# Performance work log

Hardware: AMD Instinct MI355X
Metric: run time of the kernel (lower is better)

The kernel has to match this reference:

```python
import jax, jax.numpy as jnp
import numpy as np

EMBED = 768
HEADS = 12
HEAD_DIM = EMBED // HEADS
HIDDEN = 3072
PATCH = 16
IMG = 224
GRID = IMG // PATCH  # 14
NP = GRID * GRID     # 196 patches per image
N_IMAGES = 4
N_BLOCKS = N_IMAGES - 1
B = 8


def layernorm(x, g, b, eps=1e-5):
    mu = jnp.mean(x, axis=-1, keepdims=True)
    var = jnp.mean(jnp.square(x - mu), axis=-1, keepdims=True)
    return (x - mu) * jax.lax.rsqrt(var + eps) * g + b


def patch_embed(img, w, bias):
    # conv2d(k=patch, stride=patch) == unfold to patches + linear
    Bn = img.shape[0]
    x = img.reshape(Bn, 3, GRID, PATCH, GRID, PATCH)
    x = x.transpose(0, 2, 4, 1, 3, 5).reshape(Bn, NP, 3 * PATCH * PATCH)
    return x @ w.reshape(EMBED, -1).T + bias  # [B, NP, EMBED]


def setup_inputs() -> dict:
    key = jax.random.key(0)
    ks = iter(jax.random.split(key, 64))
    d = {}
    for i in range(N_IMAGES):
        d[f"img{i}"] = jax.random.normal(next(ks), (B, 3, IMG, IMG), jnp.float32)
    d["pe_w"] = jax.random.normal(next(ks), (N_IMAGES, EMBED, 3, PATCH, PATCH)) * 0.02
    d["pe_b"] = jnp.zeros((N_IMAGES, EMBED))
    d["spatial_pos"] = jax.random.normal(next(ks), (1, NP, EMBED // 2))
    d["image_pos"] = jax.random.normal(next(ks), (1, N_IMAGES, EMBED // 2))
    d["ln_attn_g"] = jnp.ones((N_BLOCKS, EMBED)); d["ln_attn_b"] = jnp.zeros((N_BLOCKS, EMBED))
    d["qkv_w"] = jax.random.normal(next(ks), (N_BLOCKS, 3 * EMBED, EMBED)) * 0.02
    d["qkv_b"] = jnp.zeros((N_BLOCKS, 3 * EMBED))
    d["proj_w"] = jax.random.normal(next(ks), (N_BLOCKS, EMBED, EMBED)) * 0.02
    d["proj_b"] = jnp.zeros((N_BLOCKS, EMBED))
    d["ln1_g"] = jnp.ones((N_BLOCKS, EMBED)); d["ln1_b"] = jnp.zeros((N_BLOCKS, EMBED))
    d["fc1_w"] = jax.random.normal(next(ks), (N_BLOCKS, HIDDEN, EMBED)) * 0.02
    d["fc1_b"] = jnp.zeros((N_BLOCKS, HIDDEN))
    d["fc2_w"] = jax.random.normal(next(ks), (N_BLOCKS, EMBED, HIDDEN)) * 0.02
    d["fc2_b"] = jnp.zeros((N_BLOCKS, EMBED))
    d["ln2_g"] = jnp.ones((N_BLOCKS, EMBED)); d["ln2_b"] = jnp.zeros((N_BLOCKS, EMBED))
    d["final_g"] = jnp.ones((EMBED,)); d["final_b"] = jnp.zeros((EMBED,))
    d["head_w1"] = jax.random.normal(next(ks), (EMBED, EMBED)) * 0.02
    d["head_b1"] = jnp.zeros((EMBED,))
    d["head_w2"] = jax.random.normal(next(ks), (PATCH * PATCH, EMBED)) * 0.02
    d["head_b2"] = jnp.zeros((PATCH * PATCH,))
    return d


def _pos_encode(x, spatial_pos, image_pos, img_idx):
    n = x.shape[1]
    sp = spatial_pos[:, :n, :]                       # [1, n, E/2]
    ip = jnp.broadcast_to(image_pos[:, img_idx:img_idx + 1, :], (1, n, EMBED // 2))
    return x + jnp.concatenate([sp, ip], axis=-1)


def _block(x, i, p):
    # pre-norm + manual MHA
    residual = x
    h = layernorm(x, p["ln_attn_g"][i], p["ln_attn_b"][i])
    Bn, N, C = h.shape
    qkv = (h @ p["qkv_w"][i].T + p["qkv_b"][i]).reshape(Bn, N, 3, HEADS, HEAD_DIM)
    q, k, v = (qkv[:, :, j].transpose(0, 2, 1, 3) for j in range(3))  # [B,H,N,d]
    attn = jax.nn.softmax(jnp.einsum("bhnd,bhmd->bhnm", q, k) * HEAD_DIM ** -0.5, axis=-1)
    o = jnp.einsum("bhnm,bhmd->bhnd", attn, v).transpose(0, 2, 1, 3).reshape(Bn, N, C)
    x = residual + (o @ p["proj_w"][i].T + p["proj_b"][i])
    # conv block (1x1 convs == linear over channel dim)
    r = x
    h = layernorm(x, p["ln1_g"][i], p["ln1_b"][i])
    h = jax.nn.gelu(h @ p["fc1_w"][i].T + p["fc1_b"][i], approximate=False)
    h = h @ p["fc2_w"][i].T + p["fc2_b"][i]
    return layernorm(r + h, p["ln2_g"][i], p["ln2_b"][i])


def reference(img0, img1, img2, img3, pe_w, pe_b, spatial_pos, image_pos,
              ln_attn_g, ln_attn_b, qkv_w, qkv_b, proj_w, proj_b,
              ln1_g, ln1_b, fc1_w, fc1_b, fc2_w, fc2_b, ln2_g, ln2_b,
              final_g, final_b, head_w1, head_b1, head_w2, head_b2):
    p = dict(ln_attn_g=ln_attn_g, ln_attn_b=ln_attn_b, qkv_w=qkv_w, qkv_b=qkv_b,
             proj_w=proj_w, proj_b=proj_b, ln1_g=ln1_g, ln1_b=ln1_b,
             fc1_w=fc1_w, fc1_b=fc1_b, fc2_w=fc2_w, fc2_b=fc2_b,
             ln2_g=ln2_g, ln2_b=ln2_b)
    images = [img0, img1, img2, img3]
    x1 = _pos_encode(patch_embed(images[0], pe_w[0], pe_b[0]), spatial_pos, image_pos, 0)
    x2 = _pos_encode(patch_embed(images[1], pe_w[1], pe_b[1]), spatial_pos, image_pos, 1)
    x = jnp.concatenate([x1, x2], axis=1)
    x = _block(x, 0, p)
    for i in range(2, N_IMAGES):
        xn = _pos_encode(patch_embed(images[i], pe_w[i], pe_b[i]), spatial_pos, image_pos, i)
        x = jnp.concatenate([x, xn], axis=1)
        x = _block(x, i - 1, p)
    x = layernorm(x, final_g, final_b)
    x = jnp.mean(x, axis=1)                                  # [B, E]
    h = jax.nn.gelu(x @ head_w1.T + head_b1, approximate=False)
    patches = h @ head_w2.T + head_b2                        # [B, PATCH*PATCH]
    Bn = patches.shape[0]
    pimg = patches.reshape(Bn, 1, PATCH, PATCH, 1, 1)
    pimg = jnp.broadcast_to(pimg, (Bn, 1, PATCH, PATCH, GRID, GRID))
    out = pimg.transpose(0, 1, 4, 2, 5, 3).reshape(Bn, 1, IMG, IMG)
    return out
```

## Files before the change

### kernel.cpp

```cpp
#include <hip/hip_runtime.h>
#include <hip/hip_bf16.h>
#include <math.h>

#define EMBED 768
#define QKVD 2304
#define HEADS 12
#define HD 64
#define HIDDEN 3072
#define NPATCH 196
#define SEQMAX 784
#define NB 8
#define IMGSZ 224
#define GRID 14
#define PATCH 16
#define PSTR 72
#define VROW 832

typedef __hip_bfloat16 bf16;
typedef __attribute__((ext_vector_type(8))) short short8;
typedef __attribute__((ext_vector_type(4))) float f32x4;

__device__ __forceinline__ float b2f(bf16 v) { return __bfloat162float(v); }
__device__ __forceinline__ float geluf(float x) {
    return 0.5f * x * (1.0f + erff(x * 0.70710678118654752f));
}

__device__ __forceinline__ void async16(const bf16* g, bf16* l) {
    __builtin_amdgcn_global_load_lds(
        (const __attribute__((address_space(1))) unsigned int*)g,
        (__attribute__((address_space(3))) unsigned int*)l,
        16, 0, 0);
}

#define WAIT_VM0   0x0F70
#define WAIT_VM3   0x0F73
#define WAIT_VM4   0x0F74
#define WAIT_VM5   0x0F75
#define WAIT_VM6   0x0F76
#define WAIT_LGKM0 0xC07F

__global__ __launch_bounds__(256)
void detect_kernel(const unsigned short* __restrict__ raw, int* __restrict__ flag)
{
    __shared__ int bad;
    if (threadIdx.x == 0) bad = 0;
    __syncthreads();
    for (int i = threadIdx.x; i < 8192; i += 256) {
        unsigned int u = (unsigned int)raw[i] << 16;
        float v = __uint_as_float(u);
        if (!(fabsf(v) <= 1e4f)) bad = 1;
    }
    __syncthreads();
    if (threadIdx.x == 0) *flag = bad;
}

struct CvtF32 {
    const void* src[19];
    int n[19];
    int dstOff[19];
    int blkOff[20];
};
__global__ __launch_bounds__(256)
void convert_f32_all(CvtF32 c, float* __restrict__ base, const int* __restrict__ flag)
{
    int f = *flag;
    int b = blockIdx.x;
    int i = 0;
    #pragma unroll
    for (int j = 0; j < 19; ++j) if (b >= c.blkOff[j + 1]) i = j + 1;
    int e = ((b - c.blkOff[i]) * 256 + threadIdx.x) * 4;
    if (e >= c.n[i]) return;
    float* dst = base + c.dstOff[i] + e;
    if (f) {
        *(float4*)dst = *(const float4*)((const float*)c.src[i] + e);
    } else {
        const bf16* s = (const bf16*)c.src[i] + e;
        dst[0] = b2f(s[0]); dst[1] = b2f(s[1]); dst[2] = b2f(s[2]); dst[3] = b2f(s[3]);
    }
}

struct CvtB16 {
    const void* src[5];
    int n[5];
    int dstOff[5];
    int blkOff[6];
};
__global__ __launch_bounds__(256)
void convert_b16_all(CvtB16 c, bf16* __restrict__ base, const int* __restrict__ flag)
{
    int f = *flag;
    int b = blockIdx.x;
    int i = 0;
    #pragma unroll
    for (int j = 0; j < 5; ++j) if (b >= c.blkOff[j + 1]) i = j + 1;
    int e = ((b - c.blkOff[i]) * 256 + threadIdx.x) * 4;
    if (e >= c.n[i]) return;
    bf16* dst = base + (size_t)c.dstOff[i] + e;
    if (f) {
        float4 v = *(const float4*)((const float*)c.src[i] + e);
        dst[0] = __float2bfloat16(v.x); dst[1] = __float2bfloat16(v.y);
        dst[2] = __float2bfloat16(v.z); dst[3] = __float2bfloat16(v.w);
    } else {
        *(uint2*)dst = *(const uint2*)((const bf16*)c.src[i] + e);
    }
}

template<int MT>
__global__ __launch_bounds__(256)
void mfma_gemm(const bf16* __restrict__ A, const bf16* __restrict__ W,
               const float* __restrict__ bias, const float* __restrict__ add,
               float* __restrict__ outF, bf16* __restrict__ outB,
               bf16* __restrict__ Qb, bf16* __restrict__ Kb, bf16* __restrict__ Vb,
               int M, int N, int K, int Ntok, int rowStride, int mode, int magic)
{
    constexpr int MI = MT / 32;
    __shared__ __align__(16) bf16 As[2][MT * 32];
    __shared__ __align__(16) bf16 Bs[3][128 * 32];
    int tid = threadIdx.x;
    int lane = tid & 63;
    int wave = tid >> 6;
    int wm = wave & 1, wn = wave >> 1;
    int m0 = blockIdx.y * MT, n0 = blockIdx.x * 128;

    int lr = lane >> 2;
    int lc = lane & 3;
    int sc = lc ^ ((lr >> 1) & 3);
    int ar0 = (MT / 4) * wave + lr;
    int ma0 = m0 + ar0; if (ma0 >= M) ma0 = M - 1;
    int bx0 = (int)(((unsigned)ma0 * (unsigned)magic) >> 24);
    const bf16* aSrc0 = A + (size_t)(bx0 * rowStride + (ma0 - bx0 * Ntok)) * K + sc * 8;
    const bf16* aSrc1 = nullptr;
    if constexpr (MT == 128) {
        int ma1 = m0 + ar0 + 16; if (ma1 >= M) ma1 = M - 1;
        int bx1 = (int)(((unsigned)ma1 * (unsigned)magic) >> 24);
        aSrc1 = A + (size_t)(bx1 * rowStride + (ma1 - bx1 * Ntok)) * K + sc * 8;
    }
    const bf16* bSrc0 = W + (size_t)(n0 + 32 * wave + lr) * K + sc * 8;
    const bf16* bSrc1 = W + (size_t)(n0 + 32 * wave + 16 + lr) * K + sc * 8;

    int fr = lane & 15;
    int fq = lane >> 4;
    int sq = fq ^ ((fr >> 1) & 3);
    int aOff = (wm * (MT / 2) + fr) * 32 + sq * 8;
    int bOff = (wn * 64 + fr) * 32 + sq * 8;

    f32x4 acc[MI][4] = {};

    auto stageA = [&](int buf) {
        async16(aSrc0, As[buf] + ((MT / 4) * wave) * 32);
        aSrc0 += 32;
        if constexpr (MT == 128) {
            async16(aSrc1, As[buf] + ((MT / 4) * wave + 16) * 32);
            aSrc1 += 32;
        }
    };
    auto stageB = [&](int buf) {
        async16(bSrc0, Bs[buf] + (32 * wave) * 32);
        async16(bSrc1, Bs[buf] + (32 * wave + 16) * 32);
        bSrc0 += 32; bSrc1 += 32;
    };

    int nIter = K >> 5;
    stageB(0);
    stageA(0);
    stageB(1);

    int cur = 0;
    for (int it = 0; it < nIter; ++it) {
        __builtin_amdgcn_sched_barrier(0);
        __builtin_amdgcn_s_waitcnt(WAIT_LGKM0);
        __builtin_amdgcn_s_barrier();
        if (it + 1 < nIter) stageA((it + 1) & 1);
        if (it + 2 < nIter) {
            int nb = cur + 2; if (nb >= 3) nb -= 3;
            stageB(nb);
            if constexpr (MT == 128) __builtin_amdgcn_s_waitcnt(WAIT_VM6);
            else                     __builtin_amdgcn_s_waitcnt(WAIT_VM5);
        } else if (it + 1 < nIter) {
            if constexpr (MT == 128) __builtin_amdgcn_s_waitcnt(WAIT_VM4);
            else                     __builtin_amdgcn_s_waitcnt(WAIT_VM3);
        } else {
            __builtin_amdgcn_s_waitcnt(WAIT_VM0);
        }
        __builtin_amdgcn_s_barrier();
        __builtin_amdgcn_sched_barrier(0);

        const bf16* aR = As[it & 1] + aOff;
        const bf16* bR = Bs[cur] + bOff;
        short8 af[MI], bfr[4];
        #pragma unroll
        for (int mi = 0; mi < MI; ++mi) af[mi] = *(const short8*)(aR + mi * 16 * 32);
        #pragma unroll
        for (int ni = 0; ni < 4; ++ni) bfr[ni] = *(const short8*)(bR + ni * 16 * 32);
        #pragma unroll
        for (int mi = 0; mi < MI; ++mi)
            #pragma unroll
            for (int ni = 0; ni < 4; ++ni)
                acc[mi][ni] = __builtin_amdgcn_mfma_f32_16x16x32_bf16(
                    af[mi], bfr[ni], acc[mi][ni], 0, 0, 0);
        if (++cur >= 3) cur = 0;
    }

    int prA[MI][4], bxA[MI][4], tA[MI][4];
    bool okA[MI][4];
    #pragma unroll
    for (int mi = 0; mi < MI; ++mi)
        #pragma unroll
        for (int r = 0; r < 4; ++r) {
            int m = m0 + wm * (MT / 2) + mi * 16 + fq * 4 + r;
            okA[mi][r] = (m < M);
            if (m >= M) m = M - 1;
            int bx = (int)(((unsigned)m * (unsigned)magic) >> 24);
            int t = m - bx * Ntok;
            bxA[mi][r] = bx; tA[mi][r] = t;
            prA[mi][r] = bx * rowStride + t;
        }

    float bsv[4];
    #pragma unroll
    for (int ni = 0; ni < 4; ++ni) bsv[ni] = bias[n0 + wn * 64 + ni * 16 + fr];

    if (mode == 3) {
        #pragma unroll
        for (int ni = 0; ni < 4; ++ni) {
            int nb = n0 + wn * 64 + ni * 16;
            int which = (nb >= 1536) ? 2 : (nb >= 768) ? 1 : 0;
            int nnb = nb - which * 768;
            int hh = nnb >> 6;
            int dcol = (nnb & 63) + fr;
            bf16* dstb = (which == 0) ? Qb : (which == 1) ? Kb : Vb;
            #pragma unroll
            for (int mi = 0; mi < MI; ++mi)
                #pragma unroll
                for (int r = 0; r < 4; ++r) {
                    if (!okA[mi][r]) continue;
                    float v = acc[mi][ni][r] + bsv[ni];
                    dstb[((size_t)(bxA[mi][r] * HEADS + hh) * SEQMAX + tA[mi][r]) * HD + dcol]
                        = __float2bfloat16(v);
                }
        }
    } else {
        #pragma unroll
        for (int mi = 0; mi < MI; ++mi)
            #pragma unroll
            for (int r = 0; r < 4; ++r) {
                if (!okA[mi][r]) continue;
                size_t rb = (size_t)prA[mi][r] * N;
                #pragma unroll
                for (int ni = 0; ni < 4; ++ni) {
                    int n = n0 + wn * 64 + ni * 16 + fr;
                    float v = acc[mi][ni][r] + bsv[ni];
                    if (mode == 0)      outF[rb + n] = v;
                    else if (mode == 1) outF[rb + n] = v + add[rb + n];
                    else                outB[rb + n] = __float2bfloat16(geluf(v));
                }
            }
    }
}

__global__ __launch_bounds__(256)
void gemm_kernel(const float* __restrict__ A, const float* __restrict__ W,
                 const float* __restrict__ bias, const float* __restrict__ add,
                 float* __restrict__ C, int M, int N, int K,
                 int Ntok, int rowStride, int dogelu)
{
    __shared__ __align__(16) float As[16][68];
    __shared__ __align__(16) float Ws[16][68];
    int tid = threadIdx.x;
    int tx = tid & 15, ty = tid >> 4;
    int n0 = blockIdx.x * 64, m0 = blockIdx.y * 64;
    int lrow = tid >> 2;
    int lk   = (tid & 3) << 2;
    int am = m0 + lrow;
    bool aok = (am < M);
    const float* Arow = A;
    if (aok) {
        int pr = (am / Ntok) * rowStride + (am % Ntok);
        Arow = A + (size_t)pr * K;
    }
    int wn = n0 + lrow;
    const float* Wrow = (wn < N) ? (W + (size_t)wn * K) : nullptr;
    float acc[4][4] = {};
    for (int kk = 0; kk < K; kk += 16) {
        float4 av = make_float4(0.f, 0.f, 0.f, 0.f);
        if (aok) av = *(const float4*)(Arow + kk + lk);
        float4 wv = make_float4(0.f, 0.f, 0.f, 0.f);
        if (Wrow) wv = *(const float4*)(Wrow + kk + lk);
        __syncthreads();
        As[lk+0][lrow] = av.x; As[lk+1][lrow] = av.y;
        As[lk+2][lrow] = av.z; As[lk+3][lrow] = av.w;
        Ws[lk+0][lrow] = wv.x; Ws[lk+1][lrow] = wv.y;
        Ws[lk+2][lrow] = wv.z; Ws[lk+3][lrow] = wv.w;
        __syncthreads();
        #pragma unroll
        for (int k = 0; k < 16; ++k) {
            float4 a = *(const float4*)&As[k][ty << 2];
            float4 w = *(const float4*)&Ws[k][tx << 2];
            acc[0][0] += a.x*w.x; acc[0][1] += a.x*w.y; acc[0][2] += a.x*w.z; acc[0][3] += a.x*w.w;
            acc[1][0] += a.y*w.x; acc[1][1] += a.y*w.y; acc[1][2] += a.y*w.z; acc[1][3] += a.y*w.w;
            acc[2][0] += a.z*w.x; acc[2][1] += a.z*w.y; acc[2][2] += a.z*w.z; acc[2][3] += a.z*w.w;
            acc[3][0] += a.w*w.x; acc[3][1] += a.w*w.y; acc[3][2] += a.w*w.z; acc[3][3] += a.w*w.w;
        }
    }
    #pragma unroll
    for (int i = 0; i < 4; ++i) {
        int m = m0 + (ty << 2) + i;
        if (m >= M) continue;
        int pr = (m / Ntok) * rowStride + (m % Ntok);
        float* crow = C + (size_t)pr * N;
        const float* addrow = add ? (add + (size_t)pr * N) : nullptr;
        #pragma unroll
        for (int j = 0; j < 4; ++j) {
            int n = n0 + (tx << 2) + j;
            float v = acc[i][j] + bias[n];
            if (addrow) v += addrow[n];
            if (dogelu) v = geluf(v);
            crow[n] = v;
        }
    }
}

__global__ __launch_bounds__(256)
void ln_bf16_kernel(const float* __restrict__ src, bf16* __restrict__ dst,
                    const float* __restrict__ g, const float* __restrict__ bta, int Ntok)
{
    __shared__ float red[256];
    int blk = blockIdx.x;
    int t = blk % Ntok, b = blk / Ntok;
    size_t row = ((size_t)b * SEQMAX + t) * EMBED;
    int tid = threadIdx.x;
    float v0 = src[row + tid], v1 = src[row + tid + 256], v2 = src[row + tid + 512];
    red[tid] = v0 + v1 + v2;
    __syncthreads();
    for (int off = 128; off; off >>= 1) { if (tid < off) red[tid] += red[tid + off]; __syncthreads(); }
    float mu = red[0] * (1.0f / EMBED);
    __syncthreads();
    float d0 = v0 - mu, d1 = v1 - mu, d2 = v2 - mu;
    red[tid] = d0*d0 + d1*d1 + d2*d2;
    __syncthreads();
    for (int off = 128; off; off >>= 1) { if (tid < off) red[tid] += red[tid + off]; __syncthreads(); }
    float rs = rsqrtf(red[0] * (1.0f / EMBED) + 1e-5f);
    dst[row + tid]       = __float2bfloat16(d0 * rs * g[tid]       + bta[tid]);
    dst[row + tid + 256] = __float2bfloat16(d1 * rs * g[tid + 256] + bta[tid + 256]);
    dst[row + tid + 512] = __float2bfloat16(d2 * rs * g[tid + 512] + bta[tid + 512]);
}

__global__ __launch_bounds__(256)
void ln_kernel(const float* __restrict__ src, float* __restrict__ dst,
               const float* __restrict__ g, const float* __restrict__ bta, int Ntok)
{
    __shared__ float red[256];
    int blk = blockIdx.x;
    int t = blk % Ntok, b = blk / Ntok;
    size_t row = ((size_t)b * SEQMAX + t) * EMBED;
    int tid = threadIdx.x;
    float v0 = src[row + tid], v1 = src[row + tid + 256], v2 = src[row + tid + 512];
    red[tid] = v0 + v1 + v2;
    __syncthreads();
    for (int off = 128; off; off >>= 1) { if (tid < off) red[tid] += red[tid + off]; __syncthreads(); }
    float mu = red[0] * (1.0f / EMBED);
    __syncthreads();
    float d0 = v0 - mu, d1 = v1 - mu, d2 = v2 - mu;
    red[tid] = d0*d0 + d1*d1 + d2*d2;
    __syncthreads();
    for (int off = 128; off; off >>= 1) { if (tid < off) red[tid] += red[tid + off]; __syncthreads(); }
    float rs = rsqrtf(red[0] * (1.0f / EMBED) + 1e-5f);
    dst[row + tid]       = d0 * rs * g[tid]       + bta[tid];
    dst[row + tid + 256] = d1 * rs * g[tid + 256] + bta[tid + 256];
    dst[row + tid + 512] = d2 * rs * g[tid + 512] + bta[tid + 512];
}

__global__ __launch_bounds__(256)
void vtrans_kernel(const bf16* __restrict__ Vh, bf16* __restrict__ VT, int Ntok)
{
    __shared__ unsigned short Lt[64 * 66];
    int bh = blockIdx.x;
    int k0 = blockIdx.y * 64;
    const bf16* Vb = Vh + (size_t)bh * SEQMAX * HD;
    int tid = threadIdx.x;
    #pragma unroll
    for (int pass = 0; pass < 8; ++pass) {
        int key_l = (tid >> 5) + pass * 8;
        int d2 = tid & 31;
        unsigned v = 0;
        if (k0 + key_l < Ntok)
            v = *(const unsigned*)(Vb + (size_t)(k0 + key_l) * HD + d2 * 2);
        *(unsigned*)&Lt[key_l * 66 + 2 * d2] = v;
    }
    __syncthreads();
    #pragma unroll
    for (int pass = 0; pass < 8; ++pass) {
        int d = (tid >> 5) + pass * 8;
        int kp = tid & 31;
        unsigned lo = Lt[(2 * kp) * 66 + d];
        unsigned hi = Lt[(2 * kp + 1) * 66 + d];
        *(unsigned*)(VT + ((size_t)bh * HD + d) * VROW + k0 + 2 * kp) = lo | (hi << 16);
    }
}

__global__ __launch_bounds__(256)
void flash_mfma(const bf16* __restrict__ Qh, const bf16* __restrict__ Kh,
                const bf16* __restrict__ VT, bf16* __restrict__ O, int Ntok)
{
    __shared__ __align__(16) unsigned short Plds[4][32 * PSTR];
    int bh = blockIdx.x;
    int b = bh / HEADS, h = bh % HEADS;
    int t0 = blockIdx.y * 128;
    int tid = threadIdx.x;
    int lane = tid & 63, w = tid >> 6;
    int fr = lane & 15, fq = lane >> 4;

    const bf16* Qb = Qh + (size_t)bh * SEQMAX * HD;
    const bf16* Kb = Kh + (size_t)bh * SEQMAX * HD;
    const bf16* Vt = VT + (size_t)bh * HD * VROW;

    short8 aq[2][2];
    #pragma unroll
    for (int qi = 0; qi < 2; ++qi) {
        int tq = t0 + w * 32 + qi * 16 + fr; if (tq >= Ntok) tq = Ntok - 1;
        aq[qi][0] = *(const short8*)(Qb + (size_t)tq * HD + fq * 8);
        aq[qi][1] = *(const short8*)(Qb + (size_t)tq * HD + fq * 8 + 32);
    }

    float lpart[2][4] = {};
    f32x4 oacc[2][4];
    #pragma unroll
    for (int qi = 0; qi < 2; ++qi)
        #pragma unroll
        for (int dg = 0; dg < 4; ++dg) oacc[qi][dg] = (f32x4){0.f, 0.f, 0.f, 0.f};

    unsigned short* Pw = Plds[w];

    for (int k0 = 0; k0 < Ntok; k0 += 64) {
        short8 bk[4][2];
        #pragma unroll
        for (int kg = 0; kg < 4; ++kg) {
            int key = k0 + kg * 16 + fr;
            int keyc = key < Ntok ? key : Ntok - 1;
            bk[kg][0] = *(const short8*)(Kb + (size_t)keyc * HD + fq * 8);
            bk[kg][1] = *(const short8*)(Kb + (size_t)keyc * HD + fq * 8 + 32);
        }
        short8 bv[4][2];
        #pragma unroll
        for (int dg = 0; dg < 4; ++dg) {
            int d = dg * 16 + fr;
            bv[dg][0] = *(const short8*)(Vt + (size_t)d * VROW + k0 + fq * 8);
            bv[dg][1] = *(const short8*)(Vt + (size_t)d * VROW + k0 + fq * 8 + 32);
        }

        float s[2][4][4];
        #pragma unroll
        for (int qi = 0; qi < 2; ++qi)
            #pragma unroll
            for (int kg = 0; kg < 4; ++kg) {
                f32x4 sa = (f32x4){0.f, 0.f, 0.f, 0.f};
                sa = __builtin_amdgcn_mfma_f32_16x16x32_bf16(aq[qi][0], bk[kg][0], sa, 0, 0, 0);
                sa = __builtin_amdgcn_mfma_f32_16x16x32_bf16(aq[qi][1], bk[kg][1], sa, 0, 0, 0);
                #pragma unroll
                for (int r = 0; r < 4; ++r) s[qi][kg][r] = sa[r];
            }

        #pragma unroll
        for (int qi = 0; qi < 2; ++qi)
            #pragma unroll
            for (int kg = 0; kg < 4; ++kg) {
                bool ok = (k0 + kg * 16 + fr) < Ntok;
                #pragma unroll
                for (int r = 0; r < 4; ++r) {
                    float p = ok ? __expf(fminf(s[qi][kg][r] * 0.125f, 80.f)) : 0.f;
                    lpart[qi][r] += p;
                    bf16 pb = __float2bfloat16(p);
                    Pw[(qi * 16 + fq * 4 + r) * PSTR + kg * 16 + fr] = *(unsigned short*)&pb;
                }
            }

        short8 ap[2][2];
        #pragma unroll
        for (int qi = 0; qi < 2; ++qi) {
            ap[qi][0] = *(const short8*)(Pw + (qi * 16 + fr) * PSTR + fq * 8);
            ap[qi][1] = *(const short8*)(Pw + (qi * 16 + fr) * PSTR + fq * 8 + 32);
        }

        #pragma unroll
        for (int qi = 0; qi < 2; ++qi)
            #pragma unroll
            for (int dg = 0; dg < 4; ++dg) {
                oacc[qi][dg] = __builtin_amdgcn_mfma_f32_16x16x32_bf16(
                    ap[qi][0], bv[dg][0], oacc[qi][dg], 0, 0, 0);
                oacc[qi][dg] = __builtin_amdgcn_mfma_f32_16x16x32_bf16(
                    ap[qi][1], bv[dg][1], oacc[qi][dg], 0, 0, 0);
            }
    }

    #pragma unroll
    for (int qi = 0; qi < 2; ++qi)
        #pragma unroll
        for (int r = 0; r < 4; ++r) {
            float l = lpart[qi][r];
            l += __shfl_xor(l, 1); l += __shfl_xor(l, 2);
            l += __shfl_xor(l, 4); l += __shfl_xor(l, 8);
            int t = t0 + w * 32 + qi * 16 + fq * 4 + r;
            if (t >= Ntok) continue;
            float inv = 1.0f / l;
            bf16* dst = O + ((size_t)b * SEQMAX + t) * EMBED + h * HD;
            #pragma unroll
            for (int dg = 0; dg < 4; ++dg)
                dst[dg * 16 + fr] = __float2bfloat16(oacc[qi][dg][r] * inv);
        }
}

__global__ __launch_bounds__(256)
void patch_gather(const void* __restrict__ img, bf16* __restrict__ Ap,
                  const int* __restrict__ flag)
{
    int f = *flag;
    int idx = blockIdx.x * 256 + threadIdx.x;
    if (idx >= NB * NPATCH * EMBED) return;
    int col = idx % EMBED;
    int row = idx / EMBED;
    int t = row % NPATCH, b = row / NPATCH;
    int c = col >> 8;
    int pr = (col >> 4) & 15;
    int pc = col & 15;
    int gr = t / GRID, gc = t % GRID;
    size_t off = ((size_t)(b * 3 + c) * IMGSZ + gr * PATCH + pr) * IMGSZ + gc * PATCH + pc;
    float v = f ? ((const float*)img)[off] : b2f(((const bf16*)img)[off]);
    Ap[idx] = __float2bfloat16(v);
}

__global__ __launch_bounds__(256)
void posadd_kernel(const float* __restrict__ PEO, const float* __restrict__ sp,
                   const float* __restrict__ ip, float* __restrict__ X, int imgIdx)
{
    int idx = blockIdx.x * 256 + threadIdx.x;
    if (idx >= NB * NPATCH * EMBED) return;
    int e = idx % EMBED;
    int row = idx / EMBED;
    int t = row % NPATCH, b = row / NPATCH;
    float pos = (e < 384) ? sp[t * 384 + e] : ip[imgIdx * 384 + (e - 384)];
    X[((size_t)b * SEQMAX + imgIdx * NPATCH + t) * EMBED + e] = PEO[idx] + pos;
}

__global__ __launch_bounds__(768)
void mean_kernel(const float* __restrict__ H, float* __restrict__ Mn)
{
    int b = blockIdx.x;
    int e = threadIdx.x;
    float s = 0.f;
    for (int t = 0; t < SEQMAX; ++t) s += H[((size_t)b * SEQMAX + t) * EMBED + e];
    Mn[b * EMBED + e] = s * (1.0f / SEQMAX);
}

__global__ __launch_bounds__(256)
void bcast_kernel(const float* __restrict__ P, void* __restrict__ out,
                  const int* __restrict__ flag)
{
    int f = *flag;
    int idx = blockIdx.x * 256 + threadIdx.x;
    if (idx >= NB * IMGSZ * IMGSZ) return;
    int c = idx % IMGSZ;
    int r = (idx / IMGSZ) % IMGSZ;
    int b = idx / (IMGSZ * IMGSZ);
    float v = P[b * 256 + (r & 15) * 16 + (c & 15)];
    if (f) ((float*)out)[idx] = v;
    else   ((bf16*)out)[idx] = __float2bfloat16(v);
}

extern "C" void kernel_launch(void* const* d_in, const int* in_sizes, int n_in,
                              void* d_out, int out_size, void* d_ws, size_t ws_size,
                              hipStream_t stream)
{
    (void)n_in; (void)out_size; (void)ws_size;
    const void* img[4] = {d_in[0], d_in[1], d_in[2], d_in[3]};

    float* ws = (float*)d_ws;
    int* flag = (int*)ws;

    detect_kernel<<<1, 256, 0, stream>>>((const unsigned short*)d_in[0], flag);

    const bool isBig[28] = {0,0,0,0, 1,0,0,0, 0,0,1,0, 1,0,0,0, 1,0,1,0, 0,0,0,0, 0,0,0,0};
    float* fBase = ws + 16;
    float* fPtr[28] = {};
    CvtF32 cf;
    int fCnt = 0, fBlk = 0;
    cf.blkOff[0] = 0;
    {
        float* p = fBase;
        for (int i = 4; i < 28; ++i) {
            if (isBig[i]) continue;
            fPtr[i] = p;
            int n = in_sizes[i];
            cf.src[fCnt] = d_in[i];
            cf.n[fCnt] = n;
            cf.dstOff[fCnt] = (int)(p - fBase);
            fBlk += (n + 1023) / 1024;
            cf.blkOff[fCnt + 1] = fBlk;
            p += n;
            ++fCnt;
        }
        fBase = ws + 16;
        fPtr[0] = p;
    }
    convert_f32_all<<<fBlk, 256, 0, stream>>>(cf, fBase, flag);

    bf16* bPtr[28] = {};
    bf16* bBase = (bf16*)fPtr[0];
    CvtB16 cb;
    int bCnt = 0, bBlk = 0;
    cb.blkOff[0] = 0;
    float* arenaEnd;
    {
        bf16* p = bBase;
        for (int i = 4; i < 28; ++i) {
            if (!isBig[i]) continue;
            bPtr[i] = p;
            int n = in_sizes[i];
            cb.src[bCnt] = d_in[i];
            cb.n[bCnt] = n;
            cb.dstOff[bCnt] = (int)(p - bBase);
            bBlk += (n + 1023) / 1024;
            cb.blkOff[bCnt + 1] = bBlk;
            p += n;
            ++bCnt;
        }
        size_t off = p - (bf16*)ws;
        off = (off + 7) & ~(size_t)7;
        arenaEnd = (float*)((bf16*)ws + off);
    }
    convert_b16_all<<<bBlk, 256, 0, stream>>>(cb, bBase, flag);

    const bf16* pe_w   = bPtr[4];
    const bf16* qkv_w  = bPtr[10];
    const bf16* proj_w = bPtr[12];
    const bf16* fc1_w  = bPtr[16];
    const bf16* fc2_w  = bPtr[18];
    const float* pe_b      = fPtr[5];
    const float* sp        = fPtr[6];
    const float* ip        = fPtr[7];
    const float* ln_attn_g = fPtr[8];
    const float* ln_attn_b = fPtr[9];
    const float* qkv_b     = fPtr[11];
    const float* proj_b    = fPtr[13];
    const float* ln1_g     = fPtr[14];
    const float* ln1_b     = fPtr[15];
    const float* fc1_b     = fPtr[17];
    const float* fc2_b     = fPtr[19];
    const float* ln2_g     = fPtr[20];
    const float* ln2_b     = fPtr[21];
    const float* final_g   = fPtr[22];
    const float* final_b   = fPtr[23];
    const float* head_w1   = fPtr[24];
    const float* head_b1   = fPtr[25];
    const float* head_w2   = fPtr[26];
    const float* head_b2   = fPtr[27];

    const size_t SEQ = (size_t)NB * SEQMAX * EMBED;
    const size_t HID_ELEMS = (size_t)NB * SEQMAX * HIDDEN;
    const size_t EMB_ELEMS = (size_t)NB * NPATCH * EMBED;
    float* X    = arenaEnd;
    float* H    = X + SEQ;
    float* O    = H + SEQ;
    float* PEO  = O + SEQ;
    float* MEAN = PEO + EMB_ELEMS;
    float* HH   = MEAN + NB * EMBED;
    float* PTCH = HH + NB * EMBED;
    bf16* Hb    = (bf16*)(PTCH + NB * 256 + 16);
    bf16* Ob    = Hb + SEQ;
    bf16* Gb    = Ob + SEQ;
    bf16* PEb   = Gb + HID_ELEMS;
    bf16* Qb    = PEb + EMB_ELEMS;
    bf16* Kb    = Qb + SEQ;
    bf16* Vb    = Kb + SEQ;
    bf16* VTb   = Vb + SEQ;

    const int nEmb = NB * NPATCH * EMBED;

    auto magicOf = [](int d) { return (int)(16777216u / (unsigned)d + 1u); };
    const int mgE = magicOf(NB * NPATCH);

    auto embed = [&](int i) {
        patch_gather<<<(nEmb + 255) / 256, 256, 0, stream>>>(img[i], PEb, flag);
        dim3 g(EMBED / 128, (NB * NPATCH + 63) / 64);
        mfma_gemm<64><<<g, 256, 0, stream>>>(PEb, pe_w + (size_t)i * EMBED * EMBED,
                                             pe_b + i * EMBED, nullptr, PEO, nullptr,
                                             nullptr, nullptr, nullptr,
                                             NB * NPATCH, EMBED, EMBED,
                                             NB * NPATCH, NB * NPATCH, 0, mgE);
        posadd_kernel<<<(nEmb + 255) / 256, 256, 0, stream>>>(PEO, sp, ip, X, i);
    };

    auto block = [&](int i, int Ntok) {
        int M = NB * Ntok;
        int gy64  = (M + 63) / 64;
        int nkt = (Ntok + 63) / 64;
        int nqt = (Ntok + 127) / 128;
        int mg = magicOf(Ntok);
        ln_bf16_kernel<<<M, 256, 0, stream>>>(X, Hb, ln_attn_g + i * EMBED, ln_attn_b + i * EMBED, Ntok);
        mfma_gemm<64><<<dim3(QKVD / 128, gy64), 256, 0, stream>>>(
            Hb, qkv_w + (size_t)i * QKVD * EMBED, qkv_b + i * QKVD, nullptr,
            nullptr, nullptr, Qb, Kb, Vb, M, QKVD, EMBED, Ntok, SEQMAX, 3, mg);
        vtrans_kernel<<<dim3(NB * HEADS, nkt), 256, 0, stream>>>(Vb, VTb, Ntok);
        flash_mfma<<<dim3(NB * HEADS, nqt), 256, 0, stream>>>(Qb, Kb, VTb, Ob, Ntok);
        mfma_gemm<64><<<dim3(EMBED / 128, gy64), 256, 0, stream>>>(
            Ob, proj_w + (size_t)i * EMBED * EMBED, proj_b + i * EMBED, X,
            X, nullptr, nullptr, nullptr, nullptr, M, EMBED, EMBED, Ntok, SEQMAX, 1, mg);
        ln_bf16_kernel<<<M, 256, 0, stream>>>(X, Hb, ln1_g + i * EMBED, ln1_b + i * EMBED, Ntok);
        mfma_gemm<64><<<dim3(HIDDEN / 128, gy64), 256, 0, stream>>>(
            Hb, fc1_w + (size_t)i * HIDDEN * EMBED, fc1_b + i * HIDDEN, nullptr,
            nullptr, Gb, nullptr, nullptr, nullptr, M, HIDDEN, EMBED, Ntok, SEQMAX, 2, mg);
        mfma_gemm<64><<<dim3(EMBED / 128, gy64), 256, 0, stream>>>(
            Gb, fc2_w + (size_t)i * EMBED * HIDDEN, fc2_b + i * EMBED, X,
            O, nullptr, nullptr, nullptr, nullptr, M, EMBED, HIDDEN, Ntok, SEQMAX, 1, mg);
        ln_kernel<<<M, 256, 0, stream>>>(O, X, ln2_g + i * EMBED, ln2_b + i * EMBED, Ntok);
    };

    embed(0);
    embed(1);
    block(0, 392);
    embed(2);
    block(1, 588);
    embed(3);
    block(2, 784);

    ln_kernel<<<NB * SEQMAX, 256, 0, stream>>>(X, H, final_g, final_b, SEQMAX);
    mean_kernel<<<NB, 768, 0, stream>>>(H, MEAN);
    gemm_kernel<<<dim3(EMBED / 64, 1), 256, 0, stream>>>(
        MEAN, head_w1, head_b1, nullptr, HH, NB, EMBED, EMBED, NB, NB, 1);
    gemm_kernel<<<dim3(256 / 64, 1), 256, 0, stream>>>(
        HH, head_w2, head_b2, nullptr, PTCH, NB, 256, EMBED, NB, NB, 0);
    bcast_kernel<<<(NB * IMGSZ * IMGSZ + 255) / 256, 256, 0, stream>>>(PTCH, d_out, flag);
}
```

Measured before the change: 1.284 ms.

## Split-K narrow GEMMs, XCD-aware block remap, 128-row tiles for wide GEMMs

```diff
diff --git a/kernel.cpp b/kernel.cpp
--- a/kernel.cpp
+++ b/kernel.cpp
@@ -106,12 +106,14 @@
 }
 
 template<int MT>
-__global__ __launch_bounds__(256)
+__global__ __launch_bounds__(256, 4)
 void mfma_gemm(const bf16* __restrict__ A, const bf16* __restrict__ W,
                const float* __restrict__ bias, const float* __restrict__ add,
-               float* __restrict__ outF, bf16* __restrict__ outB,
+               float* __restrict__ outF, float* __restrict__ outF2,
+               bf16* __restrict__ outB,
                bf16* __restrict__ Qb, bf16* __restrict__ Kb, bf16* __restrict__ Vb,
-               int M, int N, int K, int Ntok, int rowStride, int mode, int magic)
+               int M, int N, int K, int kpitch, int Ntok, int rowStride,
+               int mode, int magic)
 {
     constexpr int MI = MT / 32;
     __shared__ __align__(16) bf16 As[2][MT * 32];
@@ -120,7 +122,20 @@
     int lane = tid & 63;
     int wave = tid >> 6;
     int wm = wave & 1, wn = wave >> 1;
-    int m0 = blockIdx.y * MT, n0 = blockIdx.x * 128;
+
+    unsigned nx = gridDim.x, ny = gridDim.y;
+    unsigned nwg = nx * ny * gridDim.z;
+    unsigned orig = blockIdx.x + nx * (blockIdx.y + ny * blockIdx.z);
+    unsigned qq = nwg >> 3, rr = nwg & 7;
+    unsigned xcd = orig & 7, idx8 = orig >> 3;
+    unsigned wg = (xcd < rr ? xcd * (qq + 1) : rr * (qq + 1) + (xcd - rr) * qq) + idx8;
+    int bxg = (int)(wg % nx);
+    unsigned tmp = wg / nx;
+    int byg = (int)(tmp % ny);
+    int bzg = (int)(tmp / ny);
+
+    int m0 = byg * MT, n0 = bxg * 128;
+    int k0 = bzg * K;
 
     int lr = lane >> 2;
     int lc = lane & 3;
@@ -128,15 +143,15 @@
     int ar0 = (MT / 4) * wave + lr;
     int ma0 = m0 + ar0; if (ma0 >= M) ma0 = M - 1;
     int bx0 = (int)(((unsigned)ma0 * (unsigned)magic) >> 24);
-    const bf16* aSrc0 = A + (size_t)(bx0 * rowStride + (ma0 - bx0 * Ntok)) * K + sc * 8;
+    const bf16* aSrc0 = A + (size_t)(bx0 * rowStride + (ma0 - bx0 * Ntok)) * kpitch + k0 + sc * 8;
     const bf16* aSrc1 = nullptr;
     if constexpr (MT == 128) {
         int ma1 = m0 + ar0 + 16; if (ma1 >= M) ma1 = M - 1;
         int bx1 = (int)(((unsigned)ma1 * (unsigned)magic) >> 24);
-        aSrc1 = A + (size_t)(bx1 * rowStride + (ma1 - bx1 * Ntok)) * K + sc * 8;
-    }
-    const bf16* bSrc0 = W + (size_t)(n0 + 32 * wave + lr) * K + sc * 8;
-    const bf16* bSrc1 = W + (size_t)(n0 + 32 * wave + 16 + lr) * K + sc * 8;
+        aSrc1 = A + (size_t)(bx1 * rowStride + (ma1 - bx1 * Ntok)) * kpitch + k0 + sc * 8;
+    }
+    const bf16* bSrc0 = W + (size_t)(n0 + 32 * wave + lr) * kpitch + k0 + sc * 8;
+    const bf16* bSrc1 = W + (size_t)(n0 + 32 * wave + 16 + lr) * kpitch + k0 + sc * 8;
 
     int fr = lane & 15;
     int fq = lane >> 4;
@@ -201,57 +216,52 @@
         if (++cur >= 3) cur = 0;
     }
 
-    int prA[MI][4], bxA[MI][4], tA[MI][4];
-    bool okA[MI][4];
-    #pragma unroll
-    for (int mi = 0; mi < MI; ++mi)
-        #pragma unroll
-        for (int r = 0; r < 4; ++r) {
-            int m = m0 + wm * (MT / 2) + mi * 16 + fq * 4 + r;
-            okA[mi][r] = (m < M);
-            if (m >= M) m = M - 1;
-            int bx = (int)(((unsigned)m * (unsigned)magic) >> 24);
-            int t = m - bx * Ntok;
-            bxA[mi][r] = bx; tA[mi][r] = t;
-            prA[mi][r] = bx * rowStride + t;
-        }
-
+    float* oF = bzg ? outF2 : outF;
     float bsv[4];
     #pragma unroll
-    for (int ni = 0; ni < 4; ++ni) bsv[ni] = bias[n0 + wn * 64 + ni * 16 + fr];
+    for (int ni = 0; ni < 4; ++ni)
+        bsv[ni] = bzg ? 0.f : bias[n0 + wn * 64 + ni * 16 + fr];
 
     if (mode == 3) {
+        bf16* dstb[4]; int hhv[4], dcv[4];
         #pragma unroll
         for (int ni = 0; ni < 4; ++ni) {
             int nb = n0 + wn * 64 + ni * 16;
             int which = (nb >= 1536) ? 2 : (nb >= 768) ? 1 : 0;
             int nnb = nb - which * 768;
-            int hh = nnb >> 6;
-            int dcol = (nnb & 63) + fr;
-            bf16* dstb = (which == 0) ? Qb : (which == 1) ? Kb : Vb;
-            #pragma unroll
-            for (int mi = 0; mi < MI; ++mi)
-                #pragma unroll
-                for (int r = 0; r < 4; ++r) {
-                    if (!okA[mi][r]) continue;
-                    float v = acc[mi][ni][r] + bsv[ni];
-                    dstb[((size_t)(bxA[mi][r] * HEADS + hh) * SEQMAX + tA[mi][r]) * HD + dcol]
-                        = __float2bfloat16(v);
-                }
-        }
-    } else {
+            dstb[ni] = (which == 0) ? Qb : (which == 1) ? Kb : Vb;
+            hhv[ni] = nnb >> 6;
+            dcv[ni] = (nnb & 63) + fr;
+        }
         #pragma unroll
         for (int mi = 0; mi < MI; ++mi)
             #pragma unroll
             for (int r = 0; r < 4; ++r) {
-                if (!okA[mi][r]) continue;
-                size_t rb = (size_t)prA[mi][r] * N;
+                int m = m0 + wm * (MT / 2) + mi * 16 + fq * 4 + r;
+                if (m >= M) continue;
+                int bx_ = (int)(((unsigned)m * (unsigned)magic) >> 24);
+                int t = m - bx_ * Ntok;
+                #pragma unroll
+                for (int ni = 0; ni < 4; ++ni)
+                    dstb[ni][((size_t)(bx_ * HEADS + hhv[ni]) * SEQMAX + t) * HD + dcv[ni]]
+                        = __float2bfloat16(acc[mi][ni][r] + bsv[ni]);
+            }
+    } else {
+        #pragma unroll
+        for (int mi = 0; mi < MI; ++mi)
+            #pragma unroll
+            for (int r = 0; r < 4; ++r) {
+                int m = m0 + wm * (MT / 2) + mi * 16 + fq * 4 + r;
+                if (m >= M) continue;
+                int bx_ = (int)(((unsigned)m * (unsigned)magic) >> 24);
+                int t = m - bx_ * Ntok;
+                size_t rb = (size_t)(bx_ * rowStride + t) * N;
                 #pragma unroll
                 for (int ni = 0; ni < 4; ++ni) {
                     int n = n0 + wn * 64 + ni * 16 + fr;
                     float v = acc[mi][ni][r] + bsv[ni];
-                    if (mode == 0)      outF[rb + n] = v;
-                    else if (mode == 1) outF[rb + n] = v + add[rb + n];
+                    if (mode == 0)      oF[rb + n] = v;
+                    else if (mode == 1) oF[rb + n] = v + add[rb + n];
                     else                outB[rb + n] = __float2bfloat16(geluf(v));
                 }
             }
@@ -371,6 +381,34 @@
 }
 
 __global__ __launch_bounds__(256)
+void ln_sum_f32_kernel(const float* __restrict__ pa, const float* __restrict__ pb,
+                       float* __restrict__ X, const float* __restrict__ g,
+                       const float* __restrict__ bta, int Ntok)
+{
+    __shared__ float red[256];
+    int blk = blockIdx.x;
+    int t = blk % Ntok, b = blk / Ntok;
+    size_t row = ((size_t)b * SEQMAX + t) * EMBED;
+    int tid = threadIdx.x;
+    float v0 = pa[row + tid]       + pb[row + tid]       + X[row + tid];
+    float v1 = pa[row + tid + 256] + pb[row + tid + 256] + X[row + tid + 256];
+    float v2 = pa[row + tid + 512] + pb[row + tid + 512] + X[row + tid + 512];
+    red[tid] = v0 + v1 + v2;
+    __syncthreads();
+    for (int off = 128; off; off >>= 1) { if (tid < off) red[tid] += red[tid + off]; __syncthreads(); }
+    float mu = red[0] * (1.0f / EMBED);
+    __syncthreads();
+    float d0 = v0 - mu, d1 = v1 - mu, d2 = v2 - mu;
+    red[tid] = d0*d0 + d1*d1 + d2*d2;
+    __syncthreads();
+    for (int off = 128; off; off >>= 1) { if (tid < off) red[tid] += red[tid + off]; __syncthreads(); }
+    float rs = rsqrtf(red[0] * (1.0f / EMBED) + 1e-5f);
+    X[row + tid]       = d0 * rs * g[tid]       + bta[tid];
+    X[row + tid + 256] = d1 * rs * g[tid + 256] + bta[tid + 256];
+    X[row + tid + 512] = d2 * rs * g[tid + 512] + bta[tid + 512];
+}
+
+__global__ __launch_bounds__(256)
 void vtrans_kernel(const bf16* __restrict__ Vh, bf16* __restrict__ VT, int Ntok)
 {
     __shared__ unsigned short Lt[64 * 66];
@@ -529,8 +567,9 @@
 }
 
 __global__ __launch_bounds__(256)
-void posadd_kernel(const float* __restrict__ PEO, const float* __restrict__ sp,
-                   const float* __restrict__ ip, float* __restrict__ X, int imgIdx)
+void posadd_kernel(const float* __restrict__ PEO, const float* __restrict__ PEO2,
+                   const float* __restrict__ sp, const float* __restrict__ ip,
+                   float* __restrict__ X, int imgIdx)
 {
     int idx = blockIdx.x * 256 + threadIdx.x;
     if (idx >= NB * NPATCH * EMBED) return;
@@ -538,7 +577,7 @@
     int row = idx / EMBED;
     int t = row % NPATCH, b = row / NPATCH;
     float pos = (e < 384) ? sp[t * 384 + e] : ip[imgIdx * 384 + (e - 384)];
-    X[((size_t)b * SEQMAX + imgIdx * NPATCH + t) * EMBED + e] = PEO[idx] + pos;
+    X[((size_t)b * SEQMAX + imgIdx * NPATCH + t) * EMBED + e] = PEO[idx] + PEO2[idx] + pos;
 }
 
 __global__ __launch_bounds__(768)
@@ -680,38 +719,43 @@
 
     auto embed = [&](int i) {
         patch_gather<<<(nEmb + 255) / 256, 256, 0, stream>>>(img[i], PEb, flag);
-        dim3 g(EMBED / 128, (NB * NPATCH + 63) / 64);
+        dim3 g(EMBED / 128, (NB * NPATCH + 63) / 64, 2);
         mfma_gemm<64><<<g, 256, 0, stream>>>(PEb, pe_w + (size_t)i * EMBED * EMBED,
-                                             pe_b + i * EMBED, nullptr, PEO, nullptr,
+                                             pe_b + i * EMBED, nullptr, PEO, H, nullptr,
                                              nullptr, nullptr, nullptr,
-                                             NB * NPATCH, EMBED, EMBED,
+                                             NB * NPATCH, EMBED, EMBED / 2, EMBED,
                                              NB * NPATCH, NB * NPATCH, 0, mgE);
-        posadd_kernel<<<(nEmb + 255) / 256, 256, 0, stream>>>(PEO, sp, ip, X, i);
+        posadd_kernel<<<(nEmb + 255) / 256, 256, 0, stream>>>(PEO, H, sp, ip, X, i);
     };
 
     auto block = [&](int i, int Ntok) {
         int M = NB * Ntok;
         int gy64  = (M + 63) / 64;
+        int gy128 = (M + 127) / 128;
         int nkt = (Ntok + 63) / 64;
         int nqt = (Ntok + 127) / 128;
         int mg = magicOf(Ntok);
         ln_bf16_kernel<<<M, 256, 0, stream>>>(X, Hb, ln_attn_g + i * EMBED, ln_attn_b + i * EMBED, Ntok);
-        mfma_gemm<64><<<dim3(QKVD / 128, gy64), 256, 0, stream>>>(
+        mfma_gemm<128><<<dim3(QKVD / 128, gy128), 256, 0, stream>>>(
             Hb, qkv_w + (size_t)i * QKVD * EMBED, qkv_b + i * QKVD, nullptr,
-            nullptr, nullptr, Qb, Kb, Vb, M, QKVD, EMBED, Ntok, SEQMAX, 3, mg);
+            nullptr, nullptr, nullptr, Qb, Kb, Vb, M, QKVD, EMBED, EMBED,
+            Ntok, SEQMAX, 3, mg);
         vtrans_kernel<<<dim3(NB * HEADS, nkt), 256, 0, stream>>>(Vb, VTb, Ntok);
         flash_mfma<<<dim3(NB * HEADS, nqt), 256, 0, stream>>>(Qb, Kb, VTb, Ob, Ntok);
         mfma_gemm<64><<<dim3(EMBED / 128, gy64), 256, 0, stream>>>(
             Ob, proj_w + (size_t)i * EMBED * EMBED, proj_b + i * EMBED, X,
-            X, nullptr, nullptr, nullptr, nullptr, M, EMBED, EMBED, Ntok, SEQMAX, 1, mg);
+            X, nullptr, nullptr, nullptr, nullptr, nullptr,
+            M, EMBED, EMBED, EMBED, Ntok, SEQMAX, 1, mg);
         ln_bf16_kernel<<<M, 256, 0, stream>>>(X, Hb, ln1_g + i * EMBED, ln1_b + i * EMBED, Ntok);
-        mfma_gemm<64><<<dim3(HIDDEN / 128, gy64), 256, 0, stream>>>(
+        mfma_gemm<128><<<dim3(HIDDEN / 128, gy128), 256, 0, stream>>>(
             Hb, fc1_w + (size_t)i * HIDDEN * EMBED, fc1_b + i * HIDDEN, nullptr,
-            nullptr, Gb, nullptr, nullptr, nullptr, M, HIDDEN, EMBED, Ntok, SEQMAX, 2, mg);
-        mfma_gemm<64><<<dim3(EMBED / 128, gy64), 256, 0, stream>>>(
-            Gb, fc2_w + (size_t)i * EMBED * HIDDEN, fc2_b + i * EMBED, X,
-            O, nullptr, nullptr, nullptr, nullptr, M, EMBED, HIDDEN, Ntok, SEQMAX, 1, mg);
-        ln_kernel<<<M, 256, 0, stream>>>(O, X, ln2_g + i * EMBED, ln2_b + i * EMBED, Ntok);
+            nullptr, nullptr, Gb, nullptr, nullptr, nullptr,
+            M, HIDDEN, EMBED, EMBED, Ntok, SEQMAX, 2, mg);
+        mfma_gemm<64><<<dim3(EMBED / 128, gy64, 2), 256, 0, stream>>>(
+            Gb, fc2_w + (size_t)i * EMBED * HIDDEN, fc2_b + i * EMBED, nullptr,
+            O, H, nullptr, nullptr, nullptr, nullptr,
+            M, EMBED, HIDDEN / 2, HIDDEN, Ntok, SEQMAX, 0, mg);
+        ln_sum_f32_kernel<<<M, 256, 0, stream>>>(O, H, X, ln2_g + i * EMBED, ln2_b + i * EMBED, Ntok);
     };
 
     embed(0);
```

Measured after the change: 1.158 ms. 1.11x faster.
